# Optimization experiments

Measured on AMD Instinct MI355X. Metric: run time of the kernel, lower is better.

## Reference

```python
import jax, jax.numpy as jnp
import numpy as np

B, S, H, NH = 2, 2048, 1024, 16
HD = H // NH  # head_dim = 64
ROPE_BASE = 10000.0


def _rope(x):
    # x: [B, NH, S, HD]; LLaMA-style half-split rotary embedding
    s, d = x.shape[2], x.shape[3]
    inv_freq = 1.0 / (ROPE_BASE ** (jnp.arange(0, d, 2, dtype=jnp.float32) / d))  # [d/2]
    ang = jnp.arange(s, dtype=jnp.float32)[:, None] * inv_freq[None, :]            # [S, d/2]
    cos, sin = jnp.cos(ang), jnp.sin(ang)
    x1, x2 = x[..., : d // 2], x[..., d // 2:]
    return jnp.concatenate([x1 * cos - x2 * sin, x1 * sin + x2 * cos], axis=-1)


def setup_inputs() -> dict:
    key = jax.random.key(0)
    ks = jax.random.split(key, 9)
    hidden_states = jax.random.normal(ks[0], (B, S, H), dtype=jnp.float32)
    # causal mask: True = attend
    causal = jnp.tril(jnp.ones((S, S), dtype=bool))
    attention_mask = jnp.broadcast_to(causal[None, None, :, :], (B, 1, S, S))
    std = 0.02
    wq = jax.random.normal(ks[1], (H, NH * HD), dtype=jnp.float32) * std
    wk = jax.random.normal(ks[2], (H, NH * HD), dtype=jnp.float32) * std
    wv = jax.random.normal(ks[3], (H, NH * HD), dtype=jnp.float32) * std
    wo = jax.random.normal(ks[4], (NH * HD, H), dtype=jnp.float32) * std
    bq = jnp.zeros((NH * HD,), dtype=jnp.float32)
    bk = jnp.zeros((NH * HD,), dtype=jnp.float32)
    bv = jnp.zeros((NH * HD,), dtype=jnp.float32)
    bo = jnp.zeros((H,), dtype=jnp.float32)
    return {"hidden_states": hidden_states, "attention_mask": attention_mask,
            "wq": wq, "bq": bq, "wk": wk, "bk": bk, "wv": wv, "bv": bv,
            "wo": wo, "bo": bo}


def _split_heads(x):
    b, s, _ = x.shape
    return jnp.transpose(x.reshape(b, s, NH, HD), (0, 2, 1, 3))


def reference(hidden_states, attention_mask, wq, bq, wk, bk, wv, bv, wo, bo):
    q = _split_heads(hidden_states @ wq + bq)  # [B,NH,S,HD]
    k = _split_heads(hidden_states @ wk + bk)
    v = _split_heads(hidden_states @ wv + bv)
    q = _rope(q)
    k = _rope(k)
    scores = jnp.einsum('bhqd,bhkd->bhqk', q, k) / jnp.sqrt(jnp.float32(HD))
    scores = jnp.where(attention_mask, scores, jnp.float32(-1e9))
    weights = jax.nn.softmax(scores, axis=-1)
    attn = jnp.einsum('bhqk,bhkv->bhqv', weights, v)  # [B,NH,S,HD]
    attn = jnp.transpose(attn, (0, 2, 1, 3)).reshape(hidden_states.shape[0], attn.shape[2], H)
    return attn @ wo + bo
```

## Files before the change

kernel.cpp:

```cpp
#include <hip/hip_runtime.h>
#include <math.h>

typedef short bf16x8 __attribute__((ext_vector_type(8)));
typedef float f32x4  __attribute__((ext_vector_type(4)));

__device__ __forceinline__ unsigned short f2bf(float f) {
    union { float f; unsigned u; } v; v.f = f;
    unsigned r = v.u + 0x7FFFu + ((v.u >> 16) & 1u);
    return (unsigned short)(r >> 16);
}

#define GLDS16(gp, lp) __builtin_amdgcn_global_load_lds( \
    (const __attribute__((address_space(1))) void*)(gp), \
    (__attribute__((address_space(3))) void*)(lp), 16, 0, 0)


__global__ __launch_bounds__(256)
void prep(const float* __restrict__ X, unsigned short* __restrict__ Xb,
          const float* __restrict__ w0, const float* __restrict__ w1,
          const float* __restrict__ w2, const float* __restrict__ w3,
          unsigned short* o0, unsigned short* o1,
          unsigned short* o2, unsigned short* o3)
{
    const int z = blockIdx.z;
    if (z >= 4) {
        const int lb = (z - 4) * 256 + blockIdx.y * 16 + blockIdx.x;
        const size_t t = (size_t)lb * 256 + threadIdx.x;
        const float4 a = *(const float4*)(X + t * 8);
        const float4 b = *(const float4*)(X + t * 8 + 4);
        unsigned short u[8] = { f2bf(a.x), f2bf(a.y), f2bf(a.z), f2bf(a.w),
                                f2bf(b.x), f2bf(b.y), f2bf(b.z), f2bf(b.w) };
        *(int4*)(Xb + t * 8) = *(int4*)u;
        return;
    }
    const float* W; unsigned short* O;
    switch (z) {
        case 0: W = w0; O = o0; break;
        case 1: W = w1; O = o1; break;
        case 2: W = w2; O = o2; break;
        default: W = w3; O = o3; break;
    }
    __shared__ float T[64][65];
    const int tid = threadIdx.x;
    const int n0 = blockIdx.x * 64, k0 = blockIdx.y * 64;
    #pragma unroll
    for (int i = 0; i < 4; i++) {
        const int k = (tid >> 4) + i * 16, n4 = (tid & 15) * 4;
        const float4 v = *(const float4*)(W + (size_t)(k0 + k) * 1024 + n0 + n4);
        T[k][n4] = v.x; T[k][n4+1] = v.y; T[k][n4+2] = v.z; T[k][n4+3] = v.w;
    }
    __syncthreads();
    if (z == 3) {
        #pragma unroll
        for (int i = 0; i < 4; i++) {
            const int n = (tid >> 4) + i * 16, k4 = (tid & 15) * 4;
            unsigned short u[4];
            #pragma unroll
            for (int j = 0; j < 4; j++) {
                const int q = k4 + j;
                const int p = (q & 3) * 16 + (q >> 2);
                const int d = (p & 3) * 16 + (p >> 2);
                u[j] = f2bf(T[d][n]);
            }
            *(int2*)(O + (size_t)(n0 + n) * 1024 + k0 + k4) = *(int2*)u;
        }
    } else {
        #pragma unroll
        for (int i = 0; i < 4; i++) {
            const int n = (tid >> 4) + i * 16, k4 = (tid & 15) * 4;
            unsigned short u[4] = { f2bf(T[k4][n]), f2bf(T[k4+1][n]),
                                    f2bf(T[k4+2][n]), f2bf(T[k4+3][n]) };
            *(int2*)(O + (size_t)(n0 + n) * 1024 + k0 + k4) = *(int2*)u;
        }
    }
}

__global__ __launch_bounds__(256)
void qkv_gemm(const unsigned short* __restrict__ Xb,
              const unsigned short* __restrict__ Wtq, const unsigned short* __restrict__ Wtk,
              const unsigned short* __restrict__ Wtv,
              const float* __restrict__ bq, const float* __restrict__ bk,
              const float* __restrict__ bv,
              unsigned short* __restrict__ Qb, unsigned short* __restrict__ Kb,
              unsigned short* __restrict__ Vtb)
{
    const unsigned short* Wt; const float* bias; unsigned short* Out;
    const int z = blockIdx.z;
    if (z == 0)      { Wt = Wtq; bias = bq; Out = Qb; }
    else if (z == 1) { Wt = Wtk; bias = bk; Out = Kb; }
    else             { Wt = Wtv; bias = bv; Out = Vtb; }

    __shared__ unsigned short Sh[128 * 72];
    unsigned short* As = Sh;
    unsigned short* Bs = Sh + 128 * 32;
    unsigned short* T  = Sh;

    const int tid = threadIdx.x, lane = tid & 63, w = tid >> 6;
    const int quad = lane >> 4, c = lane & 15;
    const int wr = w >> 1, wc = w & 1;
    const int m0 = blockIdx.x * 128, n0 = blockIdx.y * 128;
    const int srow = lane >> 2, scol = (lane & 3) * 8;

    f32x4 acc[4][4];
    #pragma unroll
    for (int i = 0; i < 4; i++)
        #pragma unroll
        for (int j = 0; j < 4; j++) acc[i][j] = (f32x4){0.f, 0.f, 0.f, 0.f};

    for (int k0 = 0; k0 < 1024; k0 += 32) {
        #pragma unroll
        for (int j = 0; j < 2; j++) {
            const int r = w * 32 + j * 16;
            GLDS16(Xb + (size_t)(m0 + r + srow) * 1024 + k0 + scol, &As[r * 32]);
            GLDS16(Wt + (size_t)(n0 + r + srow) * 1024 + k0 + scol, &Bs[r * 32]);
        }
        __syncthreads();
        bf16x8 af[4], bf[4];
        #pragma unroll
        for (int rt = 0; rt < 4; rt++)
            af[rt] = *(const bf16x8*)&As[(wr * 64 + rt * 16 + c) * 32 + quad * 8];
        #pragma unroll
        for (int nt = 0; nt < 4; nt++)
            bf[nt] = *(const bf16x8*)&Bs[(wc * 64 + nt * 16 + c) * 32 + quad * 8];
        #pragma unroll
        for (int rt = 0; rt < 4; rt++)
            #pragma unroll
            for (int nt = 0; nt < 4; nt++)
                acc[rt][nt] = __builtin_amdgcn_mfma_f32_16x16x32_bf16(af[rt], bf[nt], acc[rt][nt], 0, 0, 0);
        __syncthreads();
    }

    float bv4[4];
    #pragma unroll
    for (int nt = 0; nt < 4; nt++) bv4[nt] = bias[n0 + wc * 64 + nt * 16 + c];

    if (z == 2) {
        const int b = m0 >> 11, sb = m0 & 2047;
        const int hgbase = n0 >> 6;
        #pragma unroll
        for (int h = 0; h < 2; h++) {
            if (wc == h) {
                #pragma unroll
                for (int rt = 0; rt < 4; rt++)
                    #pragma unroll
                    for (int reg = 0; reg < 4; reg++) {
                        const int s = wr * 64 + rt * 16 + quad * 4 + reg;
                        unsigned short u[4];
                        #pragma unroll
                        for (int nt = 0; nt < 4; nt++)
                            u[nt] = f2bf(acc[rt][nt][reg] + bv4[nt]);
                        *(int2*)&T[s * 72 + c * 4] = *(int2*)u;
                    }
            }
            __syncthreads();
            const int p = tid >> 2, s8 = (tid & 3) * 32;
            unsigned short* dstb = Vtb + ((size_t)(b * 16 + hgbase + h) * 64 + p) * 2048 + sb;
            #pragma unroll
            for (int jj = 0; jj < 32; jj += 8) {
                unsigned short u[8];
                #pragma unroll
                for (int j = 0; j < 8; j++) u[j] = T[(s8 + jj + j) * 72 + p];
                *(int4*)(dstb + s8 + jj) = *(int4*)u;
            }
            __syncthreads();
        }
        return;
    }

    const float kLn = 9.210340371976184f / 32.0f;
    const float TWO_PI_INV = 0.15915494309189535f;
    const float rv0 = expf(-(float)c * kLn) * TWO_PI_INV;
    const float rv1 = expf(-(float)(c + 16) * kLn) * TWO_PI_INV;
    const float qscale = (z == 0) ? 0.125f : 1.0f;

    #pragma unroll
    for (int rt = 0; rt < 4; rt++) {
        #pragma unroll
        for (int reg = 0; reg < 4; reg++) {
            const int m = m0 + wr * 64 + rt * 16 + quad * 4 + reg;
            const int b = m >> 11, s = m & 2047;
            float x0 = acc[rt][0][reg] + bv4[0];
            float x1 = acc[rt][1][reg] + bv4[1];
            float x2 = acc[rt][2][reg] + bv4[2];
            float x3 = acc[rt][3][reg] + bv4[3];
            float r0 = (float)s * rv0;  r0 -= floorf(r0);
            float r1 = (float)s * rv1;  r1 -= floorf(r1);
            const float sn0 = __builtin_amdgcn_sinf(r0);
            const float cs0 = __builtin_amdgcn_cosf(r0);
            const float sn1 = __builtin_amdgcn_sinf(r1);
            const float cs1 = __builtin_amdgcn_cosf(r1);
            const float y0 = (x0 * cs0 - x2 * sn0) * qscale;
            const float y2 = (x0 * sn0 + x2 * cs0) * qscale;
            const float y1 = (x1 * cs1 - x3 * sn1) * qscale;
            const float y3 = (x1 * sn1 + x3 * cs1) * qscale;
            const int h = (n0 + wc * 64) >> 6;
            unsigned short u[4] = { f2bf(y0), f2bf(y1), f2bf(y2), f2bf(y3) };
            unsigned short* dst = Out + ((size_t)(b * 16 + h) * 2048 + s) * 64;
            *(int2*)(dst + c * 4) = *(int2*)u;
        }
    }
}

__global__ __launch_bounds__(256)
void out_gemm(const unsigned short* __restrict__ Ab, const unsigned short* __restrict__ Wto,
              const float* __restrict__ bo, float* __restrict__ Out)
{
    __shared__ unsigned short As[128 * 32];
    __shared__ unsigned short Bs[128 * 32];
    const int tid = threadIdx.x, lane = tid & 63, w = tid >> 6;
    const int quad = lane >> 4, c = lane & 15;
    const int wr = w >> 1, wc = w & 1;
    const int m0 = blockIdx.x * 128, n0 = blockIdx.y * 128;
    const int srow = lane >> 2, scol = (lane & 3) * 8;

    f32x4 acc[4][4];
    #pragma unroll
    for (int i = 0; i < 4; i++)
        #pragma unroll
        for (int j = 0; j < 4; j++) acc[i][j] = (f32x4){0.f, 0.f, 0.f, 0.f};

    for (int k0 = 0; k0 < 1024; k0 += 32) {
        #pragma unroll
        for (int j = 0; j < 2; j++) {
            const int r = w * 32 + j * 16;
            GLDS16(Ab  + (size_t)(m0 + r + srow) * 1024 + k0 + scol, &As[r * 32]);
            GLDS16(Wto + (size_t)(n0 + r + srow) * 1024 + k0 + scol, &Bs[r * 32]);
        }
        __syncthreads();
        bf16x8 af[4], bf[4];
        #pragma unroll
        for (int rt = 0; rt < 4; rt++)
            af[rt] = *(const bf16x8*)&As[(wr * 64 + rt * 16 + c) * 32 + quad * 8];
        #pragma unroll
        for (int nt = 0; nt < 4; nt++)
            bf[nt] = *(const bf16x8*)&Bs[(wc * 64 + nt * 16 + c) * 32 + quad * 8];
        #pragma unroll
        for (int rt = 0; rt < 4; rt++)
            #pragma unroll
            for (int nt = 0; nt < 4; nt++)
                acc[rt][nt] = __builtin_amdgcn_mfma_f32_16x16x32_bf16(af[rt], bf[nt], acc[rt][nt], 0, 0, 0);
        __syncthreads();
    }
    #pragma unroll
    for (int rt = 0; rt < 4; rt++) {
        #pragma unroll
        for (int reg = 0; reg < 4; reg++) {
            const int m = m0 + wr * 64 + rt * 16 + quad * 4 + reg;
            #pragma unroll
            for (int nt = 0; nt < 4; nt++) {
                const int n = n0 + wc * 64 + nt * 16 + c;
                Out[(size_t)m * 1024 + n] = acc[rt][nt][reg] + bo[n];
            }
        }
    }
}

__global__ __launch_bounds__(256)
void attn_part(const unsigned short* __restrict__ Qb, const unsigned short* __restrict__ Kb,
               const unsigned short* __restrict__ Vtb, unsigned short* __restrict__ Ab,
               float* __restrict__ Opart, float* __restrict__ Lpart)
{
    __shared__ unsigned short Ks[64 * 72];
    __shared__ unsigned short Vs[65 * 72];
    __shared__ unsigned short Ps[4 * 16 * 72];

    const int tid = threadIdx.x, w = tid >> 6, lane = tid & 63;
    const int quad = lane >> 4, c = lane & 15;
    const int bh = blockIdx.y;
    const int x = (blockIdx.x < 32) ? (int)blockIdx.x + 16 : (int)blockIdx.x - 32;
    int i, start, len;
    if (x < 32) { i = x + 1;  start = 0;  len = (i < 16) ? i : 16; }
    else        { i = x - 15; start = 16; len = i - 16; }
    const int q0 = (i - 1) * 64;
    const bool complete = (start == 0) && (len == i);
    const size_t base = (size_t)bh * 2048 * 64;

    if (tid < 64) Vs[64 * 72 + tid] = 0x3F80;
    __syncthreads();
    const bf16x8 on0 = *(const bf16x8*)&Vs[64 * 72 + quad * 8];
    const bf16x8 on1 = *(const bf16x8*)&Vs[64 * 72 + 32 + quad * 8];

    const int qbase = q0 + w * 16;
    const int qrow  = qbase + c;
    const size_t qoff = base + (size_t)qrow * 64;
    const bf16x8 qf0 = *(const bf16x8*)(Qb + qoff + quad * 8);
    const bf16x8 qf1 = *(const bf16x8*)(Qb + qoff + 32 + quad * 8);

    f32x4 O[4], Osum;
    Osum = (f32x4){0.f, 0.f, 0.f, 0.f};
    #pragma unroll
    for (int nt = 0; nt < 4; nt++) O[nt] = (f32x4){0.f, 0.f, 0.f, 0.f};

    const int r0s = tid >> 3, r1s = r0s + 32, c8 = (tid & 7) * 8;

    int k0 = start * 64;
    int4 kreg0 = *(const int4*)(Kb  + base + (size_t)(k0 + r0s) * 64 + c8);
    int4 kreg1 = *(const int4*)(Kb  + base + (size_t)(k0 + r1s) * 64 + c8);
    int4 vreg0 = *(const int4*)(Vtb + base + (size_t)r0s * 2048 + k0 + c8);
    int4 vreg1 = *(const int4*)(Vtb + base + (size_t)r1s * 2048 + k0 + c8);

    unsigned short* Pw = Ps + w * 16 * 72;

    for (int t = 0; t < len; t++, k0 += 64) {
        *(int4*)&Ks[(size_t)r0s * 72 + c8] = kreg0;
        *(int4*)&Ks[(size_t)r1s * 72 + c8] = kreg1;
        *(int4*)&Vs[(size_t)r0s * 72 + c8] = vreg0;
        *(int4*)&Vs[(size_t)r1s * 72 + c8] = vreg1;
        __syncthreads();

        if (t + 1 < len) {
            const int kn = k0 + 64;
            kreg0 = *(const int4*)(Kb  + base + (size_t)(kn + r0s) * 64 + c8);
            kreg1 = *(const int4*)(Kb  + base + (size_t)(kn + r1s) * 64 + c8);
            vreg0 = *(const int4*)(Vtb + base + (size_t)r0s * 2048 + kn + c8);
            vreg1 = *(const int4*)(Vtb + base + (size_t)r1s * 2048 + kn + c8);
        }

        const bool need_mask = (k0 + 63) > qbase;

        #pragma unroll
        for (int nt = 0; nt < 4; nt++) {
            const bf16x8 kf0 = *(const bf16x8*)&Ks[(nt * 16 + c) * 72 + quad * 8];
            const bf16x8 kf1 = *(const bf16x8*)&Ks[(nt * 16 + c) * 72 + 32 + quad * 8];
            f32x4 s4 = (f32x4){0.f, 0.f, 0.f, 0.f};
            s4 = __builtin_amdgcn_mfma_f32_16x16x32_bf16(kf0, qf0, s4, 0, 0, 0);
            s4 = __builtin_amdgcn_mfma_f32_16x16x32_bf16(kf1, qf1, s4, 0, 0, 0);
            const int keyb = k0 + nt * 16 + quad * 4;
            unsigned short u[4];
            #pragma unroll
            for (int reg = 0; reg < 4; reg++) {
                float p = __expf(s4[reg]);
                if (need_mask && (keyb + reg > qrow)) p = 0.f;
                u[reg] = f2bf(p);
            }
            *(int2*)&Pw[c * 72 + nt * 16 + quad * 4] = *(int2*)u;
        }

        const bf16x8 pa0 = *(const bf16x8*)&Pw[c * 72 + quad * 8];
        const bf16x8 pa1 = *(const bf16x8*)&Pw[c * 72 + 32 + quad * 8];
        #pragma unroll
        for (int nt = 0; nt < 4; nt++) {
            const bf16x8 vb0 = *(const bf16x8*)&Vs[(nt * 16 + c) * 72 + quad * 8];
            const bf16x8 vb1 = *(const bf16x8*)&Vs[(nt * 16 + c) * 72 + 32 + quad * 8];
            O[nt] = __builtin_amdgcn_mfma_f32_16x16x32_bf16(pa0, vb0, O[nt], 0, 0, 0);
            O[nt] = __builtin_amdgcn_mfma_f32_16x16x32_bf16(pa1, vb1, O[nt], 0, 0, 0);
        }
        Osum = __builtin_amdgcn_mfma_f32_16x16x32_bf16(pa0, on0, Osum, 0, 0, 0);
        Osum = __builtin_amdgcn_mfma_f32_16x16x32_bf16(pa1, on1, Osum, 0, 0, 0);
        __syncthreads();
    }

    if (complete) {
        const int b = bh >> 4, h = bh & 15;
        #pragma unroll
        for (int reg = 0; reg < 4; reg++) {
            const float inv = 1.0f / Osum[reg];
            const int q = qbase + quad * 4 + reg;
            unsigned short u[4];
            #pragma unroll
            for (int nt = 0; nt < 4; nt++) u[nt] = f2bf(O[nt][reg] * inv);
            unsigned short* dst = Ab + ((size_t)(b * 2048 + q)) * 1024 + h * 64;
            *(int2*)(dst + c * 4) = *(int2*)u;
        }
    } else {
        const int pslot = (i - 17) * 2 + (start ? 1 : 0);
        float* Op = Opart + ((size_t)bh * 32 + pslot) * 4096;
        float* Lp = Lpart + ((size_t)bh * 32 + pslot) * 64;
        #pragma unroll
        for (int reg = 0; reg < 4; reg++) {
            const int row = w * 16 + quad * 4 + reg;
            float4 o4 = make_float4(O[0][reg], O[1][reg], O[2][reg], O[3][reg]);
            *(float4*)(Op + (size_t)row * 64 + c * 4) = o4;
            if (c == 0) Lp[row] = Osum[reg];
        }
    }
}

__global__ __launch_bounds__(256)
void attn_combine(const float* __restrict__ Opart, const float* __restrict__ Lpart,
                  unsigned short* __restrict__ Ab)
{
    const int tid = threadIdx.x;
    const int j = blockIdx.x, bh = blockIdx.y;
    const int q0 = (j + 16) * 64;
    const size_t s0 = ((size_t)bh * 32 + j * 2) * 4096;
    const size_t l0 = ((size_t)bh * 32 + j * 2) * 64;

    __shared__ float linv[64];
    if (tid < 64) linv[tid] = 1.0f / (Lpart[l0 + tid] + Lpart[l0 + 64 + tid]);
    __syncthreads();

    const int row = tid >> 2, col0 = (tid & 3) * 16;
    const float inv = linv[row];
    const int b = bh >> 4, h = bh & 15;
    const int q = q0 + row;
    unsigned short* dst = Ab + ((size_t)(b * 2048 + q)) * 1024 + h * 64 + col0;
    #pragma unroll
    for (int c4 = 0; c4 < 16; c4 += 4) {
        const float4 a  = *(const float4*)(Opart + s0 + (size_t)row * 64 + col0 + c4);
        const float4 bb = *(const float4*)(Opart + s0 + 4096 + (size_t)row * 64 + col0 + c4);
        dst[c4 + 0] = f2bf((a.x + bb.x) * inv);
        dst[c4 + 1] = f2bf((a.y + bb.y) * inv);
        dst[c4 + 2] = f2bf((a.z + bb.z) * inv);
        dst[c4 + 3] = f2bf((a.w + bb.w) * inv);
    }
}

extern "C" void kernel_launch(void* const* d_in, const int* in_sizes, int n_in,
                              void* d_out, int out_size, void* d_ws, size_t ws_size,
                              hipStream_t stream)
{
    const float* X  = (const float*)d_in[0];
    const float* wq = (const float*)d_in[2];
    const float* bq = (const float*)d_in[3];
    const float* wk = (const float*)d_in[4];
    const float* bk = (const float*)d_in[5];
    const float* wv = (const float*)d_in[6];
    const float* bv = (const float*)d_in[7];
    const float* wo = (const float*)d_in[8];
    const float* bo = (const float*)d_in[9];

    unsigned short* ws = (unsigned short*)d_ws;
    const size_t M1 = 1024 * 1024;
    unsigned short* Xb  = ws;
    unsigned short* Wtq = Xb  + 4 * M1;
    unsigned short* Wtk = Wtq + M1;
    unsigned short* Wtv = Wtk + M1;
    unsigned short* Wto = Wtv + M1;
    unsigned short* Qb  = Wto + M1;
    unsigned short* Kb  = Qb  + 4 * M1;
    unsigned short* Vtb = Kb  + 4 * M1;
    unsigned short* Ab  = Vtb + 4 * M1;
    float* Opart = (float*)(Ab + 4 * M1);
    float* Lpart = Opart + (size_t)32 * 32 * 4096;

    prep        <<<dim3(16, 16, 12), 256, 0, stream>>>(X, Xb, wq, wk, wv, wo,
                                                       Wtq, Wtk, Wtv, Wto);
    qkv_gemm    <<<dim3(32, 8, 3), 256, 0, stream>>>(Xb, Wtq, Wtk, Wtv, bq, bk, bv,
                                                     Qb, Kb, Vtb);
    attn_part   <<<dim3(48, 32), 256, 0, stream>>>(Qb, Kb, Vtb, Ab, Opart, Lpart);
    attn_combine<<<dim3(16, 32), 256, 0, stream>>>(Opart, Lpart, Ab);
    out_gemm    <<<dim3(32, 8), 256, 0, stream>>>(Ab, Wto, bo, (float*)d_out);
}
```

Before: 226.1 us.

## Use 128-query attention blocks with 8 waves and shrink out_gemm M tile

The attention kernel now runs 512 threads per block covering 128 query rows, so each staged K/V tile is reused by twice as many waves. The work split moves to 24 blocks per head, with long rows split into two partial halves that a smaller combine pass merges. Waves whose queries lie entirely before a key tile skip its compute, which adds some imbalance inside the block. The output GEMM tile drops from 128 to 64 rows, doubling the grid to improve occupancy and CU coverage at the cost of less reuse of the weight tile.

```diff
diff --git a/kernel.cpp b/kernel.cpp
--- a/kernel.cpp
+++ b/kernel.cpp
@@ -205,47 +205,50 @@
 void out_gemm(const unsigned short* __restrict__ Ab, const unsigned short* __restrict__ Wto,
               const float* __restrict__ bo, float* __restrict__ Out)
 {
-    __shared__ unsigned short As[128 * 32];
+    __shared__ unsigned short As[64 * 32];
     __shared__ unsigned short Bs[128 * 32];
     const int tid = threadIdx.x, lane = tid & 63, w = tid >> 6;
     const int quad = lane >> 4, c = lane & 15;
     const int wr = w >> 1, wc = w & 1;
-    const int m0 = blockIdx.x * 128, n0 = blockIdx.y * 128;
+    const int m0 = blockIdx.x * 64, n0 = blockIdx.y * 128;
     const int srow = lane >> 2, scol = (lane & 3) * 8;
 
-    f32x4 acc[4][4];
-    #pragma unroll
-    for (int i = 0; i < 4; i++)
+    f32x4 acc[2][4];
+    #pragma unroll
+    for (int i = 0; i < 2; i++)
         #pragma unroll
         for (int j = 0; j < 4; j++) acc[i][j] = (f32x4){0.f, 0.f, 0.f, 0.f};
 
     for (int k0 = 0; k0 < 1024; k0 += 32) {
+        {
+            const int r = w * 16;
+            GLDS16(Ab + (size_t)(m0 + r + srow) * 1024 + k0 + scol, &As[r * 32]);
+        }
         #pragma unroll
         for (int j = 0; j < 2; j++) {
             const int r = w * 32 + j * 16;
-            GLDS16(Ab  + (size_t)(m0 + r + srow) * 1024 + k0 + scol, &As[r * 32]);
             GLDS16(Wto + (size_t)(n0 + r + srow) * 1024 + k0 + scol, &Bs[r * 32]);
         }
         __syncthreads();
-        bf16x8 af[4], bf[4];
-        #pragma unroll
-        for (int rt = 0; rt < 4; rt++)
-            af[rt] = *(const bf16x8*)&As[(wr * 64 + rt * 16 + c) * 32 + quad * 8];
+        bf16x8 af[2], bf[4];
+        #pragma unroll
+        for (int rt = 0; rt < 2; rt++)
+            af[rt] = *(const bf16x8*)&As[(wr * 32 + rt * 16 + c) * 32 + quad * 8];
         #pragma unroll
         for (int nt = 0; nt < 4; nt++)
             bf[nt] = *(const bf16x8*)&Bs[(wc * 64 + nt * 16 + c) * 32 + quad * 8];
         #pragma unroll
-        for (int rt = 0; rt < 4; rt++)
+        for (int rt = 0; rt < 2; rt++)
             #pragma unroll
             for (int nt = 0; nt < 4; nt++)
                 acc[rt][nt] = __builtin_amdgcn_mfma_f32_16x16x32_bf16(af[rt], bf[nt], acc[rt][nt], 0, 0, 0);
         __syncthreads();
     }
     #pragma unroll
-    for (int rt = 0; rt < 4; rt++) {
+    for (int rt = 0; rt < 2; rt++) {
         #pragma unroll
         for (int reg = 0; reg < 4; reg++) {
-            const int m = m0 + wr * 64 + rt * 16 + quad * 4 + reg;
+            const int m = m0 + wr * 32 + rt * 16 + quad * 4 + reg;
             #pragma unroll
             for (int nt = 0; nt < 4; nt++) {
                 const int n = n0 + wc * 64 + nt * 16 + c;
@@ -255,24 +258,25 @@
     }
 }
 
-__global__ __launch_bounds__(256)
+__global__ __launch_bounds__(512)
 void attn_part(const unsigned short* __restrict__ Qb, const unsigned short* __restrict__ Kb,
                const unsigned short* __restrict__ Vtb, unsigned short* __restrict__ Ab,
                float* __restrict__ Opart, float* __restrict__ Lpart)
 {
     __shared__ unsigned short Ks[64 * 72];
     __shared__ unsigned short Vs[65 * 72];
-    __shared__ unsigned short Ps[4 * 16 * 72];
+    __shared__ unsigned short Ps[8 * 16 * 72];
 
     const int tid = threadIdx.x, w = tid >> 6, lane = tid & 63;
     const int quad = lane >> 4, c = lane & 15;
     const int bh = blockIdx.y;
-    const int x = (blockIdx.x < 32) ? (int)blockIdx.x + 16 : (int)blockIdx.x - 32;
-    int i, start, len;
-    if (x < 32) { i = x + 1;  start = 0;  len = (i < 16) ? i : 16; }
-    else        { i = x - 15; start = 16; len = i - 16; }
-    const int q0 = (i - 1) * 64;
-    const bool complete = (start == 0) && (len == i);
+    const int x = blockIdx.x;
+    int ip, start, len;
+    if (x < 8)       { ip = 9 + x;  start = 0;  len = 16; }
+    else if (x < 16) { ip = 24 - x; start = 16; len = 2 * ip - 16; }
+    else             { ip = 24 - x; start = 0;  len = 2 * ip; }
+    const int q0 = (ip - 1) * 128;
+    const bool complete = (x >= 16);
     const size_t base = (size_t)bh * 2048 * 64;
 
     if (tid < 64) Vs[64 * 72 + tid] = 0x3F80;
@@ -291,62 +295,56 @@
     #pragma unroll
     for (int nt = 0; nt < 4; nt++) O[nt] = (f32x4){0.f, 0.f, 0.f, 0.f};
 
-    const int r0s = tid >> 3, r1s = r0s + 32, c8 = (tid & 7) * 8;
+    const int rs = tid >> 3, c8 = (tid & 7) * 8;
 
     int k0 = start * 64;
-    int4 kreg0 = *(const int4*)(Kb  + base + (size_t)(k0 + r0s) * 64 + c8);
-    int4 kreg1 = *(const int4*)(Kb  + base + (size_t)(k0 + r1s) * 64 + c8);
-    int4 vreg0 = *(const int4*)(Vtb + base + (size_t)r0s * 2048 + k0 + c8);
-    int4 vreg1 = *(const int4*)(Vtb + base + (size_t)r1s * 2048 + k0 + c8);
+    int4 kreg = *(const int4*)(Kb  + base + (size_t)(k0 + rs) * 64 + c8);
+    int4 vreg = *(const int4*)(Vtb + base + (size_t)rs * 2048 + k0 + c8);
 
     unsigned short* Pw = Ps + w * 16 * 72;
 
     for (int t = 0; t < len; t++, k0 += 64) {
-        *(int4*)&Ks[(size_t)r0s * 72 + c8] = kreg0;
-        *(int4*)&Ks[(size_t)r1s * 72 + c8] = kreg1;
-        *(int4*)&Vs[(size_t)r0s * 72 + c8] = vreg0;
-        *(int4*)&Vs[(size_t)r1s * 72 + c8] = vreg1;
+        *(int4*)&Ks[(size_t)rs * 72 + c8] = kreg;
+        *(int4*)&Vs[(size_t)rs * 72 + c8] = vreg;
         __syncthreads();
 
         if (t + 1 < len) {
             const int kn = k0 + 64;
-            kreg0 = *(const int4*)(Kb  + base + (size_t)(kn + r0s) * 64 + c8);
-            kreg1 = *(const int4*)(Kb  + base + (size_t)(kn + r1s) * 64 + c8);
-            vreg0 = *(const int4*)(Vtb + base + (size_t)r0s * 2048 + kn + c8);
-            vreg1 = *(const int4*)(Vtb + base + (size_t)r1s * 2048 + kn + c8);
-        }
-
-        const bool need_mask = (k0 + 63) > qbase;
-
-        #pragma unroll
-        for (int nt = 0; nt < 4; nt++) {
-            const bf16x8 kf0 = *(const bf16x8*)&Ks[(nt * 16 + c) * 72 + quad * 8];
-            const bf16x8 kf1 = *(const bf16x8*)&Ks[(nt * 16 + c) * 72 + 32 + quad * 8];
-            f32x4 s4 = (f32x4){0.f, 0.f, 0.f, 0.f};
-            s4 = __builtin_amdgcn_mfma_f32_16x16x32_bf16(kf0, qf0, s4, 0, 0, 0);
-            s4 = __builtin_amdgcn_mfma_f32_16x16x32_bf16(kf1, qf1, s4, 0, 0, 0);
-            const int keyb = k0 + nt * 16 + quad * 4;
-            unsigned short u[4];
-            #pragma unroll
-            for (int reg = 0; reg < 4; reg++) {
-                float p = __expf(s4[reg]);
-                if (need_mask && (keyb + reg > qrow)) p = 0.f;
-                u[reg] = f2bf(p);
-            }
-            *(int2*)&Pw[c * 72 + nt * 16 + quad * 4] = *(int2*)u;
-        }
-
-        const bf16x8 pa0 = *(const bf16x8*)&Pw[c * 72 + quad * 8];
-        const bf16x8 pa1 = *(const bf16x8*)&Pw[c * 72 + 32 + quad * 8];
-        #pragma unroll
-        for (int nt = 0; nt < 4; nt++) {
-            const bf16x8 vb0 = *(const bf16x8*)&Vs[(nt * 16 + c) * 72 + quad * 8];
-            const bf16x8 vb1 = *(const bf16x8*)&Vs[(nt * 16 + c) * 72 + 32 + quad * 8];
-            O[nt] = __builtin_amdgcn_mfma_f32_16x16x32_bf16(pa0, vb0, O[nt], 0, 0, 0);
-            O[nt] = __builtin_amdgcn_mfma_f32_16x16x32_bf16(pa1, vb1, O[nt], 0, 0, 0);
-        }
-        Osum = __builtin_amdgcn_mfma_f32_16x16x32_bf16(pa0, on0, Osum, 0, 0, 0);
-        Osum = __builtin_amdgcn_mfma_f32_16x16x32_bf16(pa1, on1, Osum, 0, 0, 0);
+            kreg = *(const int4*)(Kb  + base + (size_t)(kn + rs) * 64 + c8);
+            vreg = *(const int4*)(Vtb + base + (size_t)rs * 2048 + kn + c8);
+        }
+
+        if (k0 <= qbase + 15) {
+            const bool need_mask = (k0 + 63) > qbase;
+            #pragma unroll
+            for (int nt = 0; nt < 4; nt++) {
+                const bf16x8 kf0 = *(const bf16x8*)&Ks[(nt * 16 + c) * 72 + quad * 8];
+                const bf16x8 kf1 = *(const bf16x8*)&Ks[(nt * 16 + c) * 72 + 32 + quad * 8];
+                f32x4 s4 = (f32x4){0.f, 0.f, 0.f, 0.f};
+                s4 = __builtin_amdgcn_mfma_f32_16x16x32_bf16(kf0, qf0, s4, 0, 0, 0);
+                s4 = __builtin_amdgcn_mfma_f32_16x16x32_bf16(kf1, qf1, s4, 0, 0, 0);
+                const int keyb = k0 + nt * 16 + quad * 4;
+                unsigned short u[4];
+                #pragma unroll
+                for (int reg = 0; reg < 4; reg++) {
+                    float p = __expf(s4[reg]);
+                    if (need_mask && (keyb + reg > qrow)) p = 0.f;
+                    u[reg] = f2bf(p);
+                }
+                *(int2*)&Pw[c * 72 + nt * 16 + quad * 4] = *(int2*)u;
+            }
+            const bf16x8 pa0 = *(const bf16x8*)&Pw[c * 72 + quad * 8];
+            const bf16x8 pa1 = *(const bf16x8*)&Pw[c * 72 + 32 + quad * 8];
+            #pragma unroll
+            for (int nt = 0; nt < 4; nt++) {
+                const bf16x8 vb0 = *(const bf16x8*)&Vs[(nt * 16 + c) * 72 + quad * 8];
+                const bf16x8 vb1 = *(const bf16x8*)&Vs[(nt * 16 + c) * 72 + 32 + quad * 8];
+                O[nt] = __builtin_amdgcn_mfma_f32_16x16x32_bf16(pa0, vb0, O[nt], 0, 0, 0);
+                O[nt] = __builtin_amdgcn_mfma_f32_16x16x32_bf16(pa1, vb1, O[nt], 0, 0, 0);
+            }
+            Osum = __builtin_amdgcn_mfma_f32_16x16x32_bf16(pa0, on0, Osum, 0, 0, 0);
+            Osum = __builtin_amdgcn_mfma_f32_16x16x32_bf16(pa1, on1, Osum, 0, 0, 0);
+        }
         __syncthreads();
     }
 
@@ -363,9 +361,9 @@
             *(int2*)(dst + c * 4) = *(int2*)u;
         }
     } else {
-        const int pslot = (i - 17) * 2 + (start ? 1 : 0);
-        float* Op = Opart + ((size_t)bh * 32 + pslot) * 4096;
-        float* Lp = Lpart + ((size_t)bh * 32 + pslot) * 64;
+        const int pslot = (ip - 9) * 2 + (start ? 1 : 0);
+        float* Op = Opart + ((size_t)bh * 16 + pslot) * 8192;
+        float* Lp = Lpart + (size_t)bh * 2048 + (size_t)pslot * 128;
         #pragma unroll
         for (int reg = 0; reg < 4; reg++) {
             const int row = w * 16 + quad * 4 + reg;
@@ -382,23 +380,23 @@
 {
     const int tid = threadIdx.x;
     const int j = blockIdx.x, bh = blockIdx.y;
-    const int q0 = (j + 16) * 64;
-    const size_t s0 = ((size_t)bh * 32 + j * 2) * 4096;
-    const size_t l0 = ((size_t)bh * 32 + j * 2) * 64;
-
-    __shared__ float linv[64];
-    if (tid < 64) linv[tid] = 1.0f / (Lpart[l0 + tid] + Lpart[l0 + 64 + tid]);
+    const int q0 = (8 + j) * 128;
+    const size_t s0 = ((size_t)bh * 16 + j * 2) * 8192;
+    const size_t l0 = (size_t)bh * 2048 + (size_t)j * 2 * 128;
+
+    __shared__ float linv[128];
+    if (tid < 128) linv[tid] = 1.0f / (Lpart[l0 + tid] + Lpart[l0 + 128 + tid]);
     __syncthreads();
 
-    const int row = tid >> 2, col0 = (tid & 3) * 16;
+    const int row = tid >> 1, col0 = (tid & 1) * 32;
     const float inv = linv[row];
     const int b = bh >> 4, h = bh & 15;
     const int q = q0 + row;
     unsigned short* dst = Ab + ((size_t)(b * 2048 + q)) * 1024 + h * 64 + col0;
     #pragma unroll
-    for (int c4 = 0; c4 < 16; c4 += 4) {
+    for (int c4 = 0; c4 < 32; c4 += 4) {
         const float4 a  = *(const float4*)(Opart + s0 + (size_t)row * 64 + col0 + c4);
-        const float4 bb = *(const float4*)(Opart + s0 + 4096 + (size_t)row * 64 + col0 + c4);
+        const float4 bb = *(const float4*)(Opart + s0 + 8192 + (size_t)row * 64 + col0 + c4);
         dst[c4 + 0] = f2bf((a.x + bb.x) * inv);
         dst[c4 + 1] = f2bf((a.y + bb.y) * inv);
         dst[c4 + 2] = f2bf((a.z + bb.z) * inv);
@@ -432,13 +430,13 @@
     unsigned short* Vtb = Kb  + 4 * M1;
     unsigned short* Ab  = Vtb + 4 * M1;
     float* Opart = (float*)(Ab + 4 * M1);
-    float* Lpart = Opart + (size_t)32 * 32 * 4096;
+    float* Lpart = Opart + (size_t)32 * 16 * 8192;
 
     prep        <<<dim3(16, 16, 12), 256, 0, stream>>>(X, Xb, wq, wk, wv, wo,
                                                        Wtq, Wtk, Wtv, Wto);
     qkv_gemm    <<<dim3(32, 8, 3), 256, 0, stream>>>(Xb, Wtq, Wtk, Wtv, bq, bk, bv,
                                                      Qb, Kb, Vtb);
-    attn_part   <<<dim3(48, 32), 256, 0, stream>>>(Qb, Kb, Vtb, Ab, Opart, Lpart);
-    attn_combine<<<dim3(16, 32), 256, 0, stream>>>(Opart, Lpart, Ab);
-    out_gemm    <<<dim3(32, 8), 256, 0, stream>>>(Ab, Wto, bo, (float*)d_out);
-}
+    attn_part   <<<dim3(24, 32), 512, 0, stream>>>(Qb, Kb, Vtb, Ab, Opart, Lpart);
+    attn_combine<<<dim3(8, 32), 256, 0, stream>>>(Opart, Lpart, Ab);
+    out_gemm    <<<dim3(64, 8), 256, 0, stream>>>(Ab, Wto, bo, (float*)d_out);
+}
```

Measured after the change: 218.8 us. 1.03x faster.
